# Kernel optimization log

Hardware: AMD Instinct MI355X
Metric: run time of the kernel (lower is better)

The kernel has to match this reference:

```python
import jax, jax.numpy as jnp
import numpy as np

ROI = 7
EPS = 1e-3


def roi_align(images, frame_idx, boxes_px, oh, ow):
    """Bilinear RoIAlign, sampling_ratio=1 (bin centers), aligned=False.
    images: [F,C,H,W]; frame_idx: [R] int; boxes_px: [R,4] pixel coords.
    Returns [R,oh,ow,C]."""
    F_, C, H, W = images.shape
    R = boxes_px.shape[0]
    x1, y1, x2, y2 = (boxes_px[:, i] for i in range(4))
    bw = (x2 - x1) / ow
    bh = (y2 - y1) / oh
    sx = x1[:, None] + (jnp.arange(ow, dtype=boxes_px.dtype) + 0.5) * bw[:, None]  # [R,ow]
    sy = y1[:, None] + (jnp.arange(oh, dtype=boxes_px.dtype) + 0.5) * bh[:, None]  # [R,oh]
    X = jnp.broadcast_to(sx[:, None, :], (R, oh, ow))
    Y = jnp.broadcast_to(sy[:, :, None], (R, oh, ow))
    valid = (X > -1.0) & (X < W) & (Y > -1.0) & (Y < H)
    x = jnp.clip(X, 0.0, W - 1)
    y = jnp.clip(Y, 0.0, H - 1)
    x0 = jnp.floor(x).astype(jnp.int32)
    y0 = jnp.floor(y).astype(jnp.int32)
    x1i = jnp.minimum(x0 + 1, W - 1)
    y1i = jnp.minimum(y0 + 1, H - 1)
    lx = x - x0
    ly = y - y0
    f = frame_idx[:, None, None]

    def g(yy, xx):
        return images[f, :, yy, xx]  # [R,oh,ow,C]

    v = (g(y0, x0) * ((1 - ly) * (1 - lx))[..., None]
         + g(y0, x1i) * ((1 - ly) * lx)[..., None]
         + g(y1i, x0) * (ly * (1 - lx))[..., None]
         + g(y1i, x1i) * (ly * lx)[..., None])
    return v * valid[..., None].astype(v.dtype)


def bn(x, gamma, beta, mean, var):
    return (x - mean) * jax.lax.rsqrt(var + EPS) * gamma + beta


def setup_inputs() -> dict:
    key = jax.random.key(0)
    ks = jax.random.split(key, 12)
    F_, C, H, W = 64, 256, 40, 40
    N, K = 512, 8
    HID, D = 512, 512
    images = jax.random.normal(ks[0], (F_, C, H, W), jnp.float32)
    kf_indices = jax.random.randint(ks[1], (N, K), 0, F_, jnp.int32)
    u = jax.random.uniform(ks[2], (N, K, 4), jnp.float32)
    x1 = u[..., 0] * 0.6
    y1 = u[..., 1] * 0.6
    x2 = jnp.minimum(x1 + 0.2 + u[..., 2] * 0.2, 1.0)
    y2 = jnp.minimum(y1 + 0.2 + u[..., 3] * 0.2, 1.0)
    boxes = jnp.stack([x1, y1, x2, y2], axis=-1)
    fan1 = C * ROI * ROI
    w1 = jax.random.normal(ks[3], (HID, C, ROI, ROI), jnp.float32) * np.float32(np.sqrt(2.0 / fan1))
    b1 = jnp.zeros((HID,), jnp.float32)
    w2 = jax.random.normal(ks[4], (D, HID), jnp.float32) * np.float32(np.sqrt(2.0 / HID))
    b2 = jnp.zeros((D,), jnp.float32)
    g1 = jnp.ones((HID,), jnp.float32)
    bt1 = jnp.zeros((HID,), jnp.float32)
    m1 = jax.random.normal(ks[5], (HID,), jnp.float32) * 0.1
    v1 = 0.5 + jax.random.uniform(ks[6], (HID,), jnp.float32)
    g2 = jnp.ones((D,), jnp.float32)
    bt2 = jnp.zeros((D,), jnp.float32)
    m2 = jax.random.normal(ks[7], (D,), jnp.float32) * 0.1
    v2 = 0.5 + jax.random.uniform(ks[8], (D,), jnp.float32)
    return {"images": images, "kf_indices": kf_indices, "boxes": boxes,
            "w1": w1, "b1": b1, "g1": g1, "bt1": bt1, "m1": m1, "v1": v1,
            "w2": w2, "b2": b2, "g2": g2, "bt2": bt2, "m2": m2, "v2": v2}


def reference(images, kf_indices, boxes, w1, b1, g1, bt1, m1, v1, w2, b2, g2, bt2, m2, v2):
    F_, C, H, W = images.shape
    N, K = kf_indices.shape
    scale = jnp.asarray([W, H, W, H], images.dtype)
    boxes_px = (boxes * scale).reshape(N * K, 4)
    fidx = kf_indices.reshape(-1)
    roi = roi_align(images, fidx, boxes_px, ROI, ROI)        # [R,7,7,C]
    # conv1 with kernel == roi_region collapses spatial dims -> dense GEMM
    h = jnp.einsum('rhwc,ochw->ro', roi, w1) + b1            # [R,HID]
    h = jax.nn.relu(bn(h, g1, bt1, m1, v1))
    h = h @ w2.T + b2                                        # [R,D]
    h = jax.nn.relu(bn(h, g2, bt2, m2, v2))
    nodes = jnp.max(h.reshape(N, K, -1), axis=1)             # max-aggr over keyframes
    return nodes
```

## Files before the change

### kernel.cpp

```cpp
#include <hip/hip_runtime.h>


typedef __bf16 bf16x8 __attribute__((ext_vector_type(8)));
typedef float f32x4 __attribute__((ext_vector_type(4)));
typedef ushort us8v __attribute__((ext_vector_type(8)));

#define BN_EPS 1e-3f

__device__ __forceinline__ ushort f2bf(float f) {
  union { float f; unsigned u; } v; v.f = f;
  unsigned r = (v.u + 0x7FFFu + ((v.u >> 16) & 1u)) >> 16;
  return (ushort)r;
}
__device__ __forceinline__ float bf2f(ushort b) {
  union { unsigned u; float f; } v; v.u = ((unsigned)b) << 16;
  return v.f;
}
__device__ __forceinline__ void async16(const void* g, void* l) {
  __builtin_amdgcn_global_load_lds((const __attribute__((address_space(1))) void*)g,
                                   (__attribute__((address_space(3))) void*)l, 16, 0, 0);
}

__global__ __launch_bounds__(256, 6) void prep_kernel(const float* __restrict__ img,
                                                      ushort* __restrict__ imgTb,
                                                      const float* __restrict__ w1,
                                                      ushort* __restrict__ w1b,
                                                      const float* __restrict__ w2,
                                                      ushort* __restrict__ w2b,
                                                      const int* __restrict__ kf,
                                                      int* __restrict__ perm) {
  __shared__ __align__(16) char smem[25480];
  const int b = blockIdx.x;
  const int tid = threadIdx.x;
  int tIdx = -1, oIdx = -1;
  if (b < 3845) {
    int q = b / 5, r = b - q * 5;
    if (r < 4) tIdx = q * 4 + r; else oIdx = q;
  } else {
    tIdx = 3076 + (b - 3845);
  }
  if (tIdx >= 0) {
    ushort* lds = (ushort*)smem;
    const int f = tIdx / 50, p0 = (tIdx % 50) * 32;
    const float* src = img + (size_t)f * 409600 + p0;
    float4 v[2][4];
#pragma unroll
    for (int m = 0; m < 2; ++m) {
      int g = m * 256 + tid;
      int cg = g >> 3;
      int pg = g & 7;
#pragma unroll
      for (int j = 0; j < 4; ++j)
        v[m][j] = *(const float4*)(src + (size_t)(cg * 4 + j) * 1600 + pg * 4);
    }
#pragma unroll
    for (int m = 0; m < 2; ++m) {
      int g = m * 256 + tid;
      int cg = g >> 3;
      int pg = g & 7;
#pragma unroll
      for (int i = 0; i < 4; ++i) {
        ushort4 o;
        o.x = f2bf((&v[m][0].x)[i]);
        o.y = f2bf((&v[m][1].x)[i]);
        o.z = f2bf((&v[m][2].x)[i]);
        o.w = f2bf((&v[m][3].x)[i]);
        *(ushort4*)(&lds[(pg * 4 + i) * 260 + cg * 4]) = o;
      }
    }
    __syncthreads();
    ushort* dst = imgTb + ((size_t)f * 1600 + p0) * 256;
#pragma unroll
    for (int q = 0; q < 4; ++q) {
      int p = q * 8 + (tid >> 5);
      int cg8 = tid & 31;
      ushort4 a = *(const ushort4*)(&lds[p * 260 + cg8 * 8]);
      ushort4 c = *(const ushort4*)(&lds[p * 260 + cg8 * 8 + 4]);
      us8v o;
      o[0] = a.x; o[1] = a.y; o[2] = a.z; o[3] = a.w;
      o[4] = c.x; o[5] = c.y; o[6] = c.z; o[7] = c.w;
      *(us8v*)(dst + (size_t)p * 256 + cg8 * 8) = o;
    }
  } else if (oIdx < 512) {
    ushort* t = (ushort*)smem;
    const int o = oIdx;
    const float* src = w1 + (size_t)o * 12544;
    for (int j = tid; j < 12544; j += 256) {
      int c = j / 49, p = j - c * 49;
      t[p * 260 + c] = f2bf(src[j]);
    }
    __syncthreads();
    ushort* dst = w1b + (size_t)o * 12544;
    for (int k0 = tid * 8; k0 < 12544; k0 += 2048) {
      int p = k0 >> 8, c = k0 & 255;
      ushort4 a = *(const ushort4*)(&t[p * 260 + c]);
      ushort4 d = *(const ushort4*)(&t[p * 260 + c + 4]);
      us8v o8;
      o8[0] = a.x; o8[1] = a.y; o8[2] = a.z; o8[3] = a.w;
      o8[4] = d.x; o8[5] = d.y; o8[6] = d.z; o8[7] = d.w;
      *(us8v*)(dst + k0) = o8;
    }
  } else if (oIdx < 768) {
    const int o2 = oIdx - 512;
    const size_t base = (size_t)o2 * 1024 + tid * 4;
    float4 vv = *(const float4*)(w2 + base);
    ushort4 o4;
    o4.x = f2bf(vv.x); o4.y = f2bf(vv.y); o4.z = f2bf(vv.z); o4.w = f2bf(vv.w);
    *(ushort4*)(w2b + base) = o4;
  } else {
    int* cnt = (int*)smem;
    int* base = cnt + 64;
    if (tid < 64) cnt[tid] = 0;
    __syncthreads();
    for (int r = tid; r < 4096; r += 256) atomicAdd(&cnt[kf[r]], 1);
    __syncthreads();
    if (tid == 0) {
      int acc = 0;
      for (int f = 0; f < 64; ++f) { base[f] = acc; acc += cnt[f]; }
    }
    __syncthreads();
    for (int r = tid; r < 4096; r += 256) {
      int p = atomicAdd(&base[kf[r]], 1);
      perm[p] = r;
    }
  }
}

__global__ __launch_bounds__(256) void roi_kernel(const ushort* __restrict__ imgTb,
                                                  const int* __restrict__ kf,
                                                  const float* __restrict__ boxes,
                                                  const int* __restrict__ perm,
                                                  ushort* __restrict__ A) {
  __shared__ int sy0[49], sx0[49], sy1[49], sx1[49];
  __shared__ float sw00[49], sw01[49], sw10[49], sw11[49];
  __shared__ int sf, sr;
  const int tid = threadIdx.x;
  if (tid == 0) {
    int r = perm[((blockIdx.x & 7) << 9) | (blockIdx.x >> 3)];
    sr = r;
    sf = kf[r];
  }
  __syncthreads();
  const int r = sr;
  if (tid < 49) {
    int py = tid / 7, px = tid % 7;
    float x1 = boxes[r * 4 + 0] * 40.f, y1 = boxes[r * 4 + 1] * 40.f;
    float x2 = boxes[r * 4 + 2] * 40.f, y2 = boxes[r * 4 + 3] * 40.f;
    float bw = (x2 - x1) * (1.f / 7.f), bh = (y2 - y1) * (1.f / 7.f);
    float X = x1 + (px + 0.5f) * bw, Y = y1 + (py + 0.5f) * bh;
    bool valid = (X > -1.f) && (X < 40.f) && (Y > -1.f) && (Y < 40.f);
    float x = fminf(fmaxf(X, 0.f), 39.f), y = fminf(fmaxf(Y, 0.f), 39.f);
    float x0f = floorf(x), y0f = floorf(y);
    int x0 = (int)x0f, y0 = (int)y0f;
    int x1i = min(x0 + 1, 39), y1i = min(y0 + 1, 39);
    float lx = x - x0f, ly = y - y0f;
    float vm = valid ? 1.f : 0.f;
    sx0[tid] = x0; sy0[tid] = y0; sx1[tid] = x1i; sy1[tid] = y1i;
    sw00[tid] = (1.f - ly) * (1.f - lx) * vm;
    sw01[tid] = (1.f - ly) * lx * vm;
    sw10[tid] = ly * (1.f - lx) * vm;
    sw11[tid] = ly * lx * vm;
  }
  __syncthreads();
  const int c8 = (tid & 31) * 8;
  const int pq = tid >> 5;
  const ushort* base = imgTb + (size_t)sf * 409600 + c8;
  ushort* outp = A + (size_t)r * 12544 + c8;
  for (int p = pq; p < 49; p += 8) {
    const us8v a = *(const us8v*)(base + (size_t)(sy0[p] * 40 + sx0[p]) * 256);
    const us8v b = *(const us8v*)(base + (size_t)(sy0[p] * 40 + sx1[p]) * 256);
    const us8v c = *(const us8v*)(base + (size_t)(sy1[p] * 40 + sx0[p]) * 256);
    const us8v d = *(const us8v*)(base + (size_t)(sy1[p] * 40 + sx1[p]) * 256);
    float w00 = sw00[p], w01 = sw01[p], w10 = sw10[p], w11 = sw11[p];
    us8v o;
#pragma unroll
    for (int k = 0; k < 8; ++k)
      o[k] = f2bf(bf2f(a[k]) * w00 + bf2f(b[k]) * w01 + bf2f(c[k]) * w10 + bf2f(d[k]) * w11);
    *(us8v*)(outp + (size_t)p * 256) = o;
  }
}

__global__ __launch_bounds__(256, 4) void gemm1_kernel(const ushort* __restrict__ A,
                                                       const ushort* __restrict__ B,
                                                       ushort* __restrict__ P) {
  constexpr int K = 12544;
  constexpr int KS = 1792;
  __shared__ __align__(16) ushort sA[128 * 64];
  __shared__ __align__(16) ushort sB[128 * 64];
  const int tid = threadIdx.x;
  const int lane = tid & 63, wave = tid >> 6;
  const int wm = wave >> 1, wn = wave & 1;
  const int r16 = lane & 15, quad = lane >> 4;
  const int r0 = blockIdx.x * 128, c0 = blockIdx.y * 128;
  const int kStart = blockIdx.z * KS, kEnd = kStart + KS;
  const ushort* Ab = A + (size_t)r0 * K;
  const ushort* Bb = B + (size_t)c0 * K;
  const int row8 = tid >> 3;
  const int koff = (((tid & 7) ^ (row8 & 7))) * 8;
  const int sw = r16 & 7;
  f32x4 acc[4][4] = {};
  for (int kk = kStart; kk < kEnd; kk += 64) {
    __syncthreads();
#pragma unroll
    for (int s = 0; s < 4; ++s)
      async16(Ab + (size_t)(s * 32 + row8) * K + kk + koff, (char*)sA + s * 4096 + tid * 16);
#pragma unroll
    for (int s = 0; s < 4; ++s)
      async16(Bb + (size_t)(s * 32 + row8) * K + kk + koff, (char*)sB + s * 4096 + tid * 16);
    __syncthreads();
#pragma unroll
    for (int h = 0; h < 2; ++h) {
      const int slot = ((h * 4 + quad) ^ sw) * 8;
      bf16x8 af[4], bfr[4];
#pragma unroll
      for (int i = 0; i < 4; ++i)
        af[i] = *(const bf16x8*)(sA + (wm * 64 + i * 16 + r16) * 64 + slot);
#pragma unroll
      for (int j = 0; j < 4; ++j)
        bfr[j] = *(const bf16x8*)(sB + (wn * 64 + j * 16 + r16) * 64 + slot);
#pragma unroll
      for (int i = 0; i < 4; ++i)
#pragma unroll
        for (int j = 0; j < 4; ++j)
          acc[i][j] = __builtin_amdgcn_mfma_f32_16x16x32_bf16(af[i], bfr[j], acc[i][j], 0, 0, 0);
    }
  }
  ushort* Pz = P + ((size_t)blockIdx.z * 4096 + r0) * 512 + c0;
#pragma unroll
  for (int i = 0; i < 4; ++i)
#pragma unroll
    for (int j = 0; j < 4; ++j)
#pragma unroll
      for (int g = 0; g < 4; ++g)
        Pz[(size_t)(wm * 64 + i * 16 + quad * 4 + g) * 512 + (wn * 64 + j * 16 + r16)] =
            f2bf(acc[i][j][g]);
}

__global__ __launch_bounds__(256) void combine_kernel(const ushort* __restrict__ P,
                                                      const float* __restrict__ b1,
                                                      const float* __restrict__ g1,
                                                      const float* __restrict__ bt1,
                                                      const float* __restrict__ m1,
                                                      const float* __restrict__ v1,
                                                      ushort* __restrict__ h1) {
  const size_t i0 = ((size_t)blockIdx.x * 256 + threadIdx.x) * 8;
  const int col = (int)(i0 & 511);
  float x[8] = {};
#pragma unroll
  for (int z = 0; z < 7; ++z) {
    us8v pv = *(const us8v*)(P + i0 + (size_t)z * 2097152);
#pragma unroll
    for (int e = 0; e < 8; ++e) x[e] += bf2f(pv[e]);
  }
  us8v o;
#pragma unroll
  for (int e = 0; e < 8; ++e) {
    int c = col + e;
    float s = g1[c] * rsqrtf(v1[c] + BN_EPS);
    o[e] = f2bf(fmaxf((x[e] + b1[c] - m1[c]) * s + bt1[c], 0.f));
  }
  *(us8v*)(h1 + i0) = o;
}

__global__ __launch_bounds__(256) void gemm2_kernel(const ushort* __restrict__ A,
                                                    const ushort* __restrict__ B,
                                                    const float* __restrict__ b2,
                                                    const float* __restrict__ g2,
                                                    const float* __restrict__ bt2,
                                                    const float* __restrict__ m2,
                                                    const float* __restrict__ v2,
                                                    float* __restrict__ out) {
  constexpr int K = 512;
  __shared__ __align__(16) ushort sA[64 * 64];
  __shared__ __align__(16) ushort sB[128 * 64];
  __shared__ ushort st[64 * 128];
  const int tid = threadIdx.x;
  const int lane = tid & 63, wave = tid >> 6;
  const int wm = wave >> 1, wn = wave & 1;
  const int r16 = lane & 15, quad = lane >> 4;
  const int r0 = blockIdx.x * 64, c0 = blockIdx.y * 128;
  const ushort* Ab = A + (size_t)r0 * K;
  const ushort* Bb = B + (size_t)c0 * K;
  const int row8 = tid >> 3;
  const int koff = (((tid & 7) ^ (row8 & 7))) * 8;
  const int sw = r16 & 7;
  f32x4 acc[2][4] = {};
  for (int kk = 0; kk < K; kk += 64) {
    __syncthreads();
#pragma unroll
    for (int s = 0; s < 2; ++s)
      async16(Ab + (size_t)(s * 32 + row8) * K + kk + koff, (char*)sA + s * 4096 + tid * 16);
#pragma unroll
    for (int s = 0; s < 4; ++s)
      async16(Bb + (size_t)(s * 32 + row8) * K + kk + koff, (char*)sB + s * 4096 + tid * 16);
    __syncthreads();
#pragma unroll
    for (int h = 0; h < 2; ++h) {
      const int slot = ((h * 4 + quad) ^ sw) * 8;
      bf16x8 af[2], bfr[4];
#pragma unroll
      for (int i = 0; i < 2; ++i)
        af[i] = *(const bf16x8*)(sA + (wm * 32 + i * 16 + r16) * 64 + slot);
#pragma unroll
      for (int j = 0; j < 4; ++j)
        bfr[j] = *(const bf16x8*)(sB + (wn * 64 + j * 16 + r16) * 64 + slot);
#pragma unroll
      for (int i = 0; i < 2; ++i)
#pragma unroll
        for (int j = 0; j < 4; ++j)
          acc[i][j] = __builtin_amdgcn_mfma_f32_16x16x32_bf16(af[i], bfr[j], acc[i][j], 0, 0, 0);
    }
  }
  float ss[4], tt[4], bbv[4];
#pragma unroll
  for (int j = 0; j < 4; ++j) {
    int c = c0 + wn * 64 + j * 16 + r16;
    float s = g2[c] * rsqrtf(v2[c] + BN_EPS);
    ss[j] = s; tt[j] = bt2[c] - m2[c] * s; bbv[j] = b2[c];
  }
#pragma unroll
  for (int i = 0; i < 2; ++i)
#pragma unroll
    for (int j = 0; j < 4; ++j)
#pragma unroll
      for (int g = 0; g < 4; ++g) {
        int rr = wm * 32 + i * 16 + quad * 4 + g;
        int cc = wn * 64 + j * 16 + r16;
        float x = (acc[i][j][g] + bbv[j]) * ss[j] + tt[j];
        st[rr * 128 + cc] = f2bf(fmaxf(x, 0.f));
      }
  __syncthreads();
  for (int e = tid; e < 1024; e += 256) {
    int gg = e >> 7, cc = e & 127;
    float m = 0.f;
#pragma unroll
    for (int k = 0; k < 8; ++k) m = fmaxf(m, bf2f(st[(gg * 8 + k) * 128 + cc]));
    out[(size_t)(r0 / 8 + gg) * 512 + c0 + cc] = m;
  }
}

extern "C" void kernel_launch(void* const* d_in, const int* in_sizes, int n_in,
                              void* d_out, int out_size, void* d_ws, size_t ws_size,
                              hipStream_t stream) {
  (void)in_sizes; (void)n_in; (void)out_size; (void)ws_size;
  const float* images = (const float*)d_in[0];
  const int* kf      = (const int*)d_in[1];
  const float* boxes = (const float*)d_in[2];
  const float* w1    = (const float*)d_in[3];
  const float* b1    = (const float*)d_in[4];
  const float* g1    = (const float*)d_in[5];
  const float* bt1   = (const float*)d_in[6];
  const float* m1    = (const float*)d_in[7];
  const float* v1    = (const float*)d_in[8];
  const float* w2    = (const float*)d_in[9];
  const float* b2    = (const float*)d_in[10];
  const float* g2    = (const float*)d_in[11];
  const float* bt2   = (const float*)d_in[12];
  const float* m2    = (const float*)d_in[13];
  const float* v2    = (const float*)d_in[14];
  float* out = (float*)d_out;

  char* ws = (char*)d_ws;
  ushort* Abuf  = (ushort*)(ws + 0);
  ushort* w1b   = (ushort*)(ws + 102760448);
  ushort* w2b   = (ushort*)(ws + 115605504);
  ushort* imgTb = (ushort*)(ws + 116129792);
  ushort* P     = (ushort*)(ws + 116129792);
  ushort* h1    = (ushort*)(ws + 149684224);
  int*    perm  = (int*)(ws + 168558592);

  hipLaunchKernelGGL(prep_kernel, dim3(3969), dim3(256), 0, stream,
                     images, imgTb, w1, w1b, w2, w2b, kf, perm);
  hipLaunchKernelGGL(roi_kernel, dim3(4096), dim3(256), 0, stream, imgTb, kf, boxes, perm, Abuf);
  hipLaunchKernelGGL(gemm1_kernel, dim3(32, 4, 7), dim3(256), 0, stream, Abuf, w1b, P);
  hipLaunchKernelGGL(combine_kernel, dim3(1024), dim3(256), 0, stream, P, b1, g1, bt1, m1, v1, h1);
  hipLaunchKernelGGL(gemm2_kernel, dim3(64, 4), dim3(256), 0, stream, h1, w2b, b2, g2, bt2, m2, v2, out);
}
```

Measured before the change: 309.6 us.

## Pipeline gemm1 with 256x256 tiles, multi-buffered LDS and async prefetch

Rewrites the split-K GEMM1 kernel to use 256x256 output tiles with 512 threads (8 waves, each 128x64). A is double-buffered and B triple-buffered in LDS, and next-tile global-to-LDS loads are issued while MFMAs run, with explicit waitcnt, barriers and setprio. The goal is to hide global load latency and raise arithmetic intensity per loaded byte. In exchange the grid shrinks from 896 to 224 blocks, which is close to the CU count and may leave CUs idle, and register and LDS pressure increase.

```diff
diff --git a/kernel.cpp b/kernel.cpp
--- a/kernel.cpp
+++ b/kernel.cpp
@@ -180,59 +180,124 @@
   }
 }
 
-__global__ __launch_bounds__(256, 4) void gemm1_kernel(const ushort* __restrict__ A,
+__global__ __launch_bounds__(512, 2) void gemm1_kernel(const ushort* __restrict__ A,
                                                        const ushort* __restrict__ B,
                                                        ushort* __restrict__ P) {
   constexpr int K = 12544;
   constexpr int KS = 1792;
-  __shared__ __align__(16) ushort sA[128 * 64];
-  __shared__ __align__(16) ushort sB[128 * 64];
+  constexpr int NT = 28;
+  __shared__ __align__(16) ushort sA[2][16384];
+  __shared__ __align__(16) ushort sB[3][16384];
   const int tid = threadIdx.x;
   const int lane = tid & 63, wave = tid >> 6;
-  const int wm = wave >> 1, wn = wave & 1;
+  const int wm = wave >> 2, wn = wave & 3;
   const int r16 = lane & 15, quad = lane >> 4;
-  const int r0 = blockIdx.x * 128, c0 = blockIdx.y * 128;
-  const int kStart = blockIdx.z * KS, kEnd = kStart + KS;
-  const ushort* Ab = A + (size_t)r0 * K;
-  const ushort* Bb = B + (size_t)c0 * K;
+  const int sw = r16 & 7;
+  const int r0 = blockIdx.x * 256, c0 = blockIdx.y * 256;
+  const int kStart = blockIdx.z * KS;
+  const ushort* Ab = A + (size_t)r0 * K + kStart;
+  const ushort* Bb = B + (size_t)c0 * K + kStart;
   const int row8 = tid >> 3;
-  const int koff = (((tid & 7) ^ (row8 & 7))) * 8;
-  const int sw = r16 & 7;
-  f32x4 acc[4][4] = {};
-  for (int kk = kStart; kk < kEnd; kk += 64) {
-    __syncthreads();
-#pragma unroll
-    for (int s = 0; s < 4; ++s)
-      async16(Ab + (size_t)(s * 32 + row8) * K + kk + koff, (char*)sA + s * 4096 + tid * 16);
-#pragma unroll
-    for (int s = 0; s < 4; ++s)
-      async16(Bb + (size_t)(s * 32 + row8) * K + kk + koff, (char*)sB + s * 4096 + tid * 16);
-    __syncthreads();
-#pragma unroll
-    for (int h = 0; h < 2; ++h) {
-      const int slot = ((h * 4 + quad) ^ sw) * 8;
-      bf16x8 af[4], bfr[4];
-#pragma unroll
-      for (int i = 0; i < 4; ++i)
-        af[i] = *(const bf16x8*)(sA + (wm * 64 + i * 16 + r16) * 64 + slot);
+  const int koff = ((tid & 7) ^ (row8 & 7)) * 8;
+  f32x4 acc[8][4] = {};
+
+#pragma unroll
+  for (int s = 0; s < 4; ++s)
+    async16(Ab + (size_t)(s * 64 + row8) * K + koff, (char*)sA[0] + s * 8192 + tid * 16);
+#pragma unroll
+  for (int s = 0; s < 4; ++s)
+    async16(Bb + (size_t)(s * 64 + row8) * K + koff, (char*)sB[0] + s * 8192 + tid * 16);
+#pragma unroll
+  for (int s = 0; s < 4; ++s)
+    async16(Bb + (size_t)(s * 64 + row8) * K + 64 + koff, (char*)sB[1] + s * 8192 + tid * 16);
+  asm volatile("s_waitcnt vmcnt(4)" ::: "memory");
+  __builtin_amdgcn_sched_barrier(0);
+  __builtin_amdgcn_s_barrier();
+
+  int Bcur = 0;
+  for (int kt = 0; kt < NT; ++kt) {
+    const int Acur = kt & 1;
+    const ushort* a_base = sA[Acur];
+    const ushort* b_base = sB[Bcur];
+    bf16x8 bfr[4][2], af[4][2];
+#pragma unroll
+    for (int j = 0; j < 4; ++j)
+#pragma unroll
+      for (int h = 0; h < 2; ++h)
+        bfr[j][h] = *(const bf16x8*)(b_base + (wn * 64 + j * 16 + r16) * 64 +
+                                     ((h * 4 + quad) ^ sw) * 8);
+#pragma unroll
+    for (int i = 0; i < 4; ++i)
+#pragma unroll
+      for (int h = 0; h < 2; ++h)
+        af[i][h] = *(const bf16x8*)(a_base + (wm * 128 + i * 16 + r16) * 64 +
+                                    ((h * 4 + quad) ^ sw) * 8);
+    if (kt + 1 < NT) {
+      const int kk1 = (kt + 1) * 64;
+#pragma unroll
+      for (int s = 0; s < 4; ++s)
+        async16(Ab + (size_t)(s * 64 + row8) * K + kk1 + koff,
+                (char*)sA[Acur ^ 1] + s * 8192 + tid * 16);
+    }
+    __builtin_amdgcn_s_barrier();
+    asm volatile("s_waitcnt lgkmcnt(0)" ::: "memory");
+    __builtin_amdgcn_sched_barrier(0);
+    __builtin_amdgcn_s_setprio(1);
+#pragma unroll
+    for (int i = 0; i < 4; ++i)
 #pragma unroll
       for (int j = 0; j < 4; ++j)
-        bfr[j] = *(const bf16x8*)(sB + (wn * 64 + j * 16 + r16) * 64 + slot);
-#pragma unroll
-      for (int i = 0; i < 4; ++i)
-#pragma unroll
-        for (int j = 0; j < 4; ++j)
-          acc[i][j] = __builtin_amdgcn_mfma_f32_16x16x32_bf16(af[i], bfr[j], acc[i][j], 0, 0, 0);
-    }
-  }
+#pragma unroll
+        for (int h = 0; h < 2; ++h)
+          acc[i][j] =
+              __builtin_amdgcn_mfma_f32_16x16x32_bf16(af[i][h], bfr[j][h], acc[i][j], 0, 0, 0);
+    __builtin_amdgcn_s_setprio(0);
+    __builtin_amdgcn_s_barrier();
+#pragma unroll
+    for (int i = 0; i < 4; ++i)
+#pragma unroll
+      for (int h = 0; h < 2; ++h)
+        af[i][h] = *(const bf16x8*)(a_base + (wm * 128 + (i + 4) * 16 + r16) * 64 +
+                                    ((h * 4 + quad) ^ sw) * 8);
+    if (kt + 2 < NT) {
+      int b2 = Bcur + 2; if (b2 >= 3) b2 -= 3;
+      const int kk2 = (kt + 2) * 64;
+#pragma unroll
+      for (int s = 0; s < 4; ++s)
+        async16(Bb + (size_t)(s * 64 + row8) * K + kk2 + koff,
+                (char*)sB[b2] + s * 8192 + tid * 16);
+    }
+    __builtin_amdgcn_s_barrier();
+    asm volatile("s_waitcnt lgkmcnt(0)" ::: "memory");
+    __builtin_amdgcn_sched_barrier(0);
+    __builtin_amdgcn_s_setprio(1);
+#pragma unroll
+    for (int i = 0; i < 4; ++i)
+#pragma unroll
+      for (int j = 0; j < 4; ++j)
+#pragma unroll
+        for (int h = 0; h < 2; ++h)
+          acc[i + 4][j] = __builtin_amdgcn_mfma_f32_16x16x32_bf16(af[i][h], bfr[j][h],
+                                                                  acc[i + 4][j], 0, 0, 0);
+    __builtin_amdgcn_s_setprio(0);
+    if (kt + 2 < NT) {
+      asm volatile("s_waitcnt vmcnt(4)" ::: "memory");
+    } else {
+      asm volatile("s_waitcnt vmcnt(0)" ::: "memory");
+    }
+    __builtin_amdgcn_sched_barrier(0);
+    __builtin_amdgcn_s_barrier();
+    Bcur = (Bcur + 1 == 3) ? 0 : Bcur + 1;
+  }
+
   ushort* Pz = P + ((size_t)blockIdx.z * 4096 + r0) * 512 + c0;
 #pragma unroll
-  for (int i = 0; i < 4; ++i)
+  for (int i = 0; i < 8; ++i)
 #pragma unroll
     for (int j = 0; j < 4; ++j)
 #pragma unroll
       for (int g = 0; g < 4; ++g)
-        Pz[(size_t)(wm * 64 + i * 16 + quad * 4 + g) * 512 + (wn * 64 + j * 16 + r16)] =
+        Pz[(size_t)(wm * 128 + i * 16 + quad * 4 + g) * 512 + (wn * 64 + j * 16 + r16)] =
             f2bf(acc[i][j][g]);
 }
 
@@ -372,7 +437,7 @@
   hipLaunchKernelGGL(prep_kernel, dim3(3969), dim3(256), 0, stream,
                      images, imgTb, w1, w1b, w2, w2b, kf, perm);
   hipLaunchKernelGGL(roi_kernel, dim3(4096), dim3(256), 0, stream, imgTb, kf, boxes, perm, Abuf);
-  hipLaunchKernelGGL(gemm1_kernel, dim3(32, 4, 7), dim3(256), 0, stream, Abuf, w1b, P);
+  hipLaunchKernelGGL(gemm1_kernel, dim3(16, 2, 7), dim3(512), 0, stream, Abuf, w1b, P);
   hipLaunchKernelGGL(combine_kernel, dim3(1024), dim3(256), 0, stream, P, b1, g1, bt1, m1, v1, h1);
   hipLaunchKernelGGL(gemm2_kernel, dim3(64, 4), dim3(256), 0, stream, h1, w2b, b2, g2, bt2, m2, v2, out);
 }
```

After: 306.1 us, median of 2. About the same (-1.1%).
